# Kernel optimization log

Measured on AMD Instinct MI355X. Metric: run time of the kernel, lower is better.

The kernel has to match this reference:

```python
import jax, jax.numpy as jnp
import numpy as np

DIM = 64
HID = 32  # dim * 1/2
P = 4     # patch_size

def _conv1x1(x, w):
    # x: [B,C,H,W], w: [O,C] -> [B,O,H,W]
    return jnp.einsum('oc,bchw->bohw', w, x)

def _dwconv3x3(x, w):
    # depthwise 3x3, padding 1. x: [B,C,H,W], w: [C,1,3,3]
    return jax.lax.conv_general_dilated(
        x, w, window_strides=(1, 1), padding=((1, 1), (1, 1)),
        dimension_numbers=('NCHW', 'OIHW', 'NCHW'),
        feature_group_count=x.shape[1])

def setup_inputs() -> dict:
    key = jax.random.key(0)
    k1, k2, k3, k4 = jax.random.split(key, 4)
    B, H, W = 4, 512, 512
    x = jax.random.normal(k1, (B, DIM, H, W), dtype=jnp.float32)
    w_in1 = jax.random.normal(k2, (2 * HID, DIM), dtype=jnp.float32) * 0.05
    w_dw = jax.random.normal(k3, (2 * HID, 1, 3, 3), dtype=jnp.float32) * 0.1
    w_in2 = jax.random.normal(k4, (DIM, HID), dtype=jnp.float32) * 0.05
    w_freq = jnp.ones((DIM, 1, 1, P, P // 2 + 1), dtype=jnp.float32)
    return {'x': x, 'w_in1': w_in1, 'w_dw': w_dw, 'w_in2': w_in2, 'w_freq': w_freq}

def reference(x, w_in1, w_dw, w_in2, w_freq):
    shortcut = x
    y = _dwconv3x3(_conv1x1(x, w_in1), w_dw)          # [B,2*HID,H,W]
    y1, y2 = jnp.split(y, 2, axis=1)
    y = jax.nn.gelu(y1, approximate=False) * y2       # [B,HID,H,W]
    y = _conv1x1(y, w_in2)                            # [B,DIM,H,W]
    b, c, h, w = y.shape
    h_n = (P - h % P) % P
    w_n = (P - w % P) % P
    if h_n or w_n:
        y = jnp.pad(y, ((0, 0), (0, 0), (0, h_n), (0, w_n)), mode='reflect')
    hp, wp = y.shape[2] // P, y.shape[3] // P
    # [B,C,hp,P,wp,P] -> [B,C,hp,wp,P,P]
    yp = y.reshape(b, c, hp, P, wp, P).transpose(0, 1, 2, 4, 3, 5)
    yf = jnp.fft.rfft2(yp)                            # [B,C,hp,wp,P,P//2+1] complex
    yf = w_freq * yf                                  # w_freq broadcasts over (C,1,1,P,P//2+1)
    yp = jnp.fft.irfft2(yf, s=(P, P))
    y = yp.transpose(0, 1, 2, 4, 3, 5).reshape(b, c, hp * P, wp * P)
    y = y[:, :, :h, :w]
    return y + shortcut
```

## Files before the change

kernel.cpp:

```cpp
#include <hip/hip_runtime.h>
#include <math.h>

#define DIMC 64
#define HIDC 32
#define IMH 512
#define IMW 512
#define NBATCH 4
#define TW 32
#define TH 8
#define HW 34
#define HH 10
#define NPIX (HW*HH)
#define NPIXP 352
#define NCHUNK 22
#define TSTRIDE 35
#define VSTRIDE 17
#define PLANE (IMH*IMW)

typedef short short8 __attribute__((ext_vector_type(8)));
typedef float f32x4  __attribute__((ext_vector_type(4)));

static __device__ __forceinline__ unsigned cvt_pk_bf16(float lo, float hi) {
    unsigned r;
    asm("v_cvt_pk_bf16_f32 %0, %1, %2" : "=v"(r) : "v"(lo), "v"(hi));
    return r;
}
static __device__ __forceinline__ float bf2f_lo(unsigned s) {
    union { unsigned u; float f; } v; v.u = s << 16; return v.f;
}
static __device__ __forceinline__ float bf2f_hi(unsigned s) {
    union { unsigned u; float f; } v; v.u = s & 0xffff0000u; return v.f;
}
static __device__ __forceinline__ unsigned f2bf(float f) {
    union { float f; unsigned u; } v; v.f = f;
    return (v.u + 0x7fffu + ((v.u >> 16) & 1u)) >> 16;
}

static __device__ __forceinline__ float gelu_f(float u) {
    const float z  = fabsf(u) * 0.70710678118654752f;
    const float t  = __builtin_amdgcn_rcpf(fmaf(0.3275911f, z, 1.0f));
    const float e  = __builtin_amdgcn_exp2f(-z * z * 1.4426950408889634f);
    float p = fmaf(t, 1.061405429f, -1.453152027f);
    p = fmaf(t, p, 1.421413741f);
    p = fmaf(t, p, -0.284496736f);
    p = fmaf(t, p, 0.254829592f);
    p = p * t;
    const float erf_abs = fmaf(-p, e, 1.0f);
    const float erfv = copysignf(erf_abs, u);
    return 0.5f * u * (1.0f + erfv);
}

__global__ __launch_bounds__(256, 3)
void ffn_fused_kernel(const float* __restrict__ x,
                      const float* __restrict__ w1,
                      const float* __restrict__ wdw,
                      const float* __restrict__ w2,
                      const float* __restrict__ wf,
                      float* __restrict__ out)
{
    __shared__ unsigned ts[NPIXP * TSTRIDE];
    __shared__ int s_ident;

    const int tid = threadIdx.x;
    const int bid = ((blockIdx.x & 7) << 9) + (blockIdx.x >> 3);
    const int b  = bid >> 10;
    const int tr = bid & 1023;
    const int ty = tr >> 4, tx = tr & 15;
    const int oy = ty * TH, ox = tx * TW;

    if (tid == 0) s_ident = 1;
    __syncthreads();
    if (tid < DIMC) {
        bool idf = true;
        #pragma unroll
        for (int k = 0; k < 12; ++k) idf = idf && (wf[tid * 12 + k] == 1.0f);
        if (!idf) atomicAnd(&s_ident, 0);
    }

    const float* xb = x + (size_t)b * DIMC * PLANE;

    for (int p = tid; p < NPIXP; p += 256) {
        const int hy = p / HW, hx = p % HW;
        const int gy = oy + hy - 1, gx = ox + hx - 1;
        unsigned* row = &ts[p * TSTRIDE];
        if (p >= NPIX || (unsigned)gy >= IMH || (unsigned)gx >= IMW) {
            #pragma unroll
            for (int w = 0; w < 32; ++w) row[w] = 0u;
        } else {
            const float* xp = xb + (size_t)gy * IMW + gx;
            #pragma unroll
            for (int c0 = 0; c0 < DIMC; c0 += 8) {
                float f[8];
                #pragma unroll
                for (int i = 0; i < 8; ++i) f[i] = xp[(size_t)(c0 + i) * PLANE];
                #pragma unroll
                for (int i = 0; i < 8; i += 2)
                    row[(c0 + i) >> 1] = cvt_pk_bf16(f[i], f[i + 1]);
            }
        }
    }

    const int lane = tid & 63, wid = tid >> 6;
    const int l15 = lane & 15, lg = lane >> 4;

    short8 afrag1[4][2];
    #pragma unroll
    for (int mt = 0; mt < 4; ++mt) {
        #pragma unroll
        for (int ks = 0; ks < 2; ++ks) {
            const float* wp = w1 + (size_t)(mt * 16 + l15) * DIMC + ks * 32 + lg * 8;
            f32x4 wa = *reinterpret_cast<const f32x4*>(wp);
            f32x4 wb = *reinterpret_cast<const f32x4*>(wp + 4);
            union { unsigned u[4]; short8 s; } pk;
            pk.u[0] = cvt_pk_bf16(wa[0], wa[1]); pk.u[1] = cvt_pk_bf16(wa[2], wa[3]);
            pk.u[2] = cvt_pk_bf16(wb[0], wb[1]); pk.u[3] = cvt_pk_bf16(wb[2], wb[3]);
            afrag1[mt][ks] = pk.s;
        }
    }
    short8 afrag2[4];
    #pragma unroll
    for (int mt = 0; mt < 4; ++mt) {
        const float* wp = w2 + (size_t)(mt * 16 + l15) * HIDC + lg * 8;
        f32x4 wa = *reinterpret_cast<const f32x4*>(wp);
        f32x4 wb = *reinterpret_cast<const f32x4*>(wp + 4);
        union { unsigned u[4]; short8 s; } pk;
        pk.u[0] = cvt_pk_bf16(wa[0], wa[1]); pk.u[1] = cvt_pk_bf16(wa[2], wa[3]);
        pk.u[2] = cvt_pk_bf16(wb[0], wb[1]); pk.u[3] = cvt_pk_bf16(wb[2], wb[3]);
        afrag2[mt] = pk.s;
    }
    __syncthreads();

    unsigned xs[4][4][2];
    #pragma unroll
    for (int cc = 0; cc < 4; ++cc) {
        const int px = wid * 64 + cc * 16 + l15;
        const unsigned hp = (unsigned)(((px >> 5) + 1) * HW + (px & 31) + 1) * TSTRIDE;
        #pragma unroll
        for (int mt = 0; mt < 4; ++mt) {
            xs[cc][mt][0] = ts[hp + mt * 8 + lg * 2];
            xs[cc][mt][1] = ts[hp + mt * 8 + lg * 2 + 1];
        }
    }
    __syncthreads();

    for (int chunk = wid; chunk < NCHUNK; chunk += 4) {
        const unsigned base = (unsigned)(chunk * 16 + l15) * TSTRIDE;
        f32x4 acc[4];
        #pragma unroll
        for (int mt = 0; mt < 4; ++mt) acc[mt] = (f32x4)0.0f;
        #pragma unroll
        for (int ks = 0; ks < 2; ++ks) {
            union { unsigned u[4]; short8 s; } bw;
            #pragma unroll
            for (int t = 0; t < 4; ++t) bw.u[t] = ts[base + ks * 16 + lg * 4 + t];
            #pragma unroll
            for (int mt = 0; mt < 4; ++mt)
                acc[mt] = __builtin_amdgcn_mfma_f32_16x16x32_bf16(afrag1[mt][ks], bw.s, acc[mt], 0, 0, 0);
        }
        #pragma unroll
        for (int mt = 0; mt < 2; ++mt) {
            #pragma unroll
            for (int r = 0; r < 4; ++r)
                ts[base + mt * 16 + lg * 4 + r] = cvt_pk_bf16(acc[mt][r], acc[mt + 2][r]);
        }
    }
    __syncthreads();

    const int li = tid >> 5, lj = tid & 31;
    unsigned vpack[16];
    #pragma unroll 2
    for (int c2 = 0; c2 < 16; ++c2) {
        const int ca = 2 * c2, cb = 2 * c2 + 1;
        float u1a = 0.0f, u2a = 0.0f, u1b = 0.0f, u2b = 0.0f;
        #pragma unroll
        for (int di = 0; di < 3; ++di) {
            #pragma unroll
            for (int dj = 0; dj < 3; ++dj) {
                const int k = di * 3 + dj;
                const unsigned base = ((li + di) * HW + (lj + dj)) * TSTRIDE + ca;
                const unsigned ua = ts[base];
                const unsigned ub = ts[base + 1];
                u1a = fmaf(wdw[ca * 9 + k],          bf2f_lo(ua), u1a);
                u2a = fmaf(wdw[(ca + HIDC) * 9 + k], bf2f_hi(ua), u2a);
                u1b = fmaf(wdw[cb * 9 + k],          bf2f_lo(ub), u1b);
                u2b = fmaf(wdw[(cb + HIDC) * 9 + k], bf2f_hi(ub), u2b);
            }
        }
        const float va = gelu_f(u1a) * u2a;
        const float vb = gelu_f(u1b) * u2b;
        vpack[c2] = cvt_pk_bf16(va, vb);
    }
    __syncthreads();

    unsigned* vls = ts;
    {
        const unsigned vb_ = (unsigned)tid * VSTRIDE;
        #pragma unroll
        for (int w = 0; w < 16; ++w) vls[vb_ + w] = vpack[w];
    }
    __syncthreads();

    float* ob = out + (size_t)b * DIMC * PLANE;
    if (s_ident) {
        #pragma unroll
        for (int cc = 0; cc < 4; ++cc) {
            const int chunk = wid * 4 + cc;
            const int px = chunk * 16 + l15;
            union { unsigned u[4]; short8 s; } bw;
            #pragma unroll
            for (int t = 0; t < 4; ++t) bw.u[t] = vls[(unsigned)px * VSTRIDE + lg * 4 + t];
            const size_t pix = (size_t)(oy + (px >> 5)) * IMW + (ox + (px & 31));
            float* op = ob + pix;
            #pragma unroll
            for (int mt = 0; mt < 4; ++mt) {
                f32x4 acc = __builtin_amdgcn_mfma_f32_16x16x32_bf16(afrag2[mt], bw.s, (f32x4)0.0f, 0, 0, 0);
                #pragma unroll
                for (int r = 0; r < 4; ++r) {
                    const int ch = mt * 16 + lg * 4 + r;
                    const unsigned xw = xs[cc][mt][r >> 1];
                    const float xv = (r & 1) ? bf2f_hi(xw) : bf2f_lo(xw);
                    op[(size_t)ch * PLANE] = acc[r] + xv;
                }
            }
        }
    } else {
        float* ys = (float*)(ts + 8192);
        for (int mt = 0; mt < 4; ++mt) {
            __syncthreads();
            #pragma unroll
            for (int cc = 0; cc < 4; ++cc) {
                const int chunk = wid * 4 + cc;
                const int px = chunk * 16 + l15;
                union { unsigned u[4]; short8 s; } bw;
                #pragma unroll
                for (int t = 0; t < 4; ++t) bw.u[t] = vls[(unsigned)px * VSTRIDE + lg * 4 + t];
                f32x4 acc = __builtin_amdgcn_mfma_f32_16x16x32_bf16(afrag2[mt], bw.s, (f32x4)0.0f, 0, 0, 0);
                #pragma unroll
                for (int r = 0; r < 4; ++r)
                    ys[(lg * 4 + r) * 257 + px] = acc[r];
            }
            __syncthreads();
            {
                const int chl = tid >> 4;
                const int ch  = mt * 16 + chl;
                const int pt  = tid & 15;
                const int pi = (pt >> 3) * 4, pj = (pt & 7) * 4;
                float yv[4][4];
                #pragma unroll
                for (int a = 0; a < 4; ++a)
                    #pragma unroll
                    for (int c = 0; c < 4; ++c)
                        yv[a][c] = ys[chl * 257 + (pi + a) * TW + (pj + c)];
                float Cr[4][4], Ci[4][4];
                #pragma unroll
                for (int j = 0; j < 4; ++j) {
                    const float s02 = yv[0][j] + yv[2][j], d02 = yv[0][j] - yv[2][j];
                    const float s13 = yv[1][j] + yv[3][j], d13 = yv[1][j] - yv[3][j];
                    Cr[0][j] = s02 + s13; Ci[0][j] = 0.0f;
                    Cr[1][j] = d02;       Ci[1][j] = -d13;
                    Cr[2][j] = s02 - s13; Ci[2][j] = 0.0f;
                    Cr[3][j] = d02;       Ci[3][j] = d13;
                }
                float Zr[4][3], Zi[4][3];
                #pragma unroll
                for (int u = 0; u < 4; ++u) {
                    const float r0 = Cr[u][0], r1 = Cr[u][1], r2 = Cr[u][2], r3 = Cr[u][3];
                    const float i0 = Ci[u][0], i1 = Ci[u][1], i2 = Ci[u][2], i3 = Ci[u][3];
                    Zr[u][0] = r0 + r1 + r2 + r3;     Zi[u][0] = i0 + i1 + i2 + i3;
                    Zr[u][1] = (r0 - r2) + (i1 - i3); Zi[u][1] = (i0 - i2) - (r1 - r3);
                    Zr[u][2] = r0 - r1 + r2 - r3;     Zi[u][2] = i0 - i1 + i2 - i3;
                    #pragma unroll
                    for (int vv = 0; vv < 3; ++vv) {
                        const float m = wf[ch * 12 + u * 3 + vv];
                        Zr[u][vv] *= m; Zi[u][vv] *= m;
                    }
                }
                float Ar[4][3], Ai[4][3];
                #pragma unroll
                for (int vv = 0; vv < 3; ++vv) {
                    const float r0 = Zr[0][vv], r1 = Zr[1][vv], r2 = Zr[2][vv], r3 = Zr[3][vv];
                    const float i0 = Zi[0][vv], i1 = Zi[1][vv], i2 = Zi[2][vv], i3 = Zi[3][vv];
                    Ar[0][vv] = r0 + r1 + r2 + r3;     Ai[0][vv] = i0 + i1 + i2 + i3;
                    Ar[1][vv] = (r0 - r2) - (i1 - i3); Ai[1][vv] = (i0 - i2) + (r1 - r3);
                    Ar[2][vv] = r0 - r1 + r2 - r3;     Ai[2][vv] = i0 - i1 + i2 - i3;
                    Ar[3][vv] = (r0 - r2) + (i1 - i3); Ai[3][vv] = (i0 - i2) - (r1 - r3);
                }
                const float* xc = xb + (size_t)ch * PLANE;
                float*       oc = ob + (size_t)ch * PLANE;
                #pragma unroll
                for (int a = 0; a < 4; ++a) {
                    const float A0 = Ar[a][0], A1r = Ar[a][1], A2 = Ar[a][2];
                    const float B1i = Ai[a][1];
                    float res[4];
                    res[0] = (A0 + 2.0f * A1r + A2) * 0.0625f;
                    res[1] = (A0 - 2.0f * B1i - A2) * 0.0625f;
                    res[2] = (A0 - 2.0f * A1r + A2) * 0.0625f;
                    res[3] = (A0 + 2.0f * B1i - A2) * 0.0625f;
                    #pragma unroll
                    for (int c = 0; c < 4; ++c) {
                        const size_t pix = (size_t)(oy + pi + a) * IMW + (ox + pj + c);
                        oc[pix] = res[c] + xc[pix];
                    }
                }
            }
        }
    }
}

extern "C" void kernel_launch(void* const* d_in, const int* in_sizes, int n_in,
                              void* d_out, int out_size, void* d_ws, size_t ws_size,
                              hipStream_t stream) {
    (void)in_sizes; (void)n_in; (void)d_ws; (void)ws_size; (void)out_size;
    const float* x   = (const float*)d_in[0];
    const float* w1  = (const float*)d_in[1];
    const float* wdw = (const float*)d_in[2];
    const float* w2  = (const float*)d_in[3];
    const float* wf  = (const float*)d_in[4];
    float* out = (float*)d_out;

    const int blocks = NBATCH * (IMH / TH) * (IMW / TW);
    ffn_fused_kernel<<<blocks, 256, 0, stream>>>(x, w1, wdw, w2, wf, out);
}
```

Measured before the change: 212.9 us.

## Switch to fp16 packed math, taller tiles, XOR-swizzled LDS and weight prep kernel

Moves the intermediate data from bf16 to fp16 and runs the depthwise 3x3 with packed half2 FMAs instead of scalar fp32 FMAs. The tile height doubles to 16 rows with 512-thread blocks, which cuts the halo recompute overhead. The padded LDS stride is replaced by an XOR swizzle so 128-bit LDS accesses can be used. A small prep kernel pre-packs weights and the identity flag into the workspace. The risks are fp16 range and precision loss in the accumulation, an extra kernel launch, and higher LDS per block, which may lower occupancy.

New measurement: 191.0 us. 10.3% less time.

```diff
diff --git a/kernel.cpp b/kernel.cpp
--- a/kernel.cpp
+++ b/kernel.cpp
@@ -1,39 +1,48 @@
 #include <hip/hip_runtime.h>
+#include <hip/hip_fp16.h>
 #include <math.h>
 
 #define DIMC 64
 #define HIDC 32
 #define IMH 512
 #define IMW 512
-#define NBATCH 4
 #define TW 32
-#define TH 8
+#define TH 16
 #define HW 34
-#define HH 10
+#define HH 18
 #define NPIX (HW*HH)
-#define NPIXP 352
-#define NCHUNK 22
-#define TSTRIDE 35
-#define VSTRIDE 17
+#define NPIXP 624
+#define NCHUNK 39
 #define PLANE (IMH*IMW)
 
-typedef short short8 __attribute__((ext_vector_type(8)));
-typedef float f32x4  __attribute__((ext_vector_type(4)));
-
-static __device__ __forceinline__ unsigned cvt_pk_bf16(float lo, float hi) {
-    unsigned r;
-    asm("v_cvt_pk_bf16_f32 %0, %1, %2" : "=v"(r) : "v"(lo), "v"(hi));
-    return r;
-}
-static __device__ __forceinline__ float bf2f_lo(unsigned s) {
-    union { unsigned u; float f; } v; v.u = s << 16; return v.f;
-}
-static __device__ __forceinline__ float bf2f_hi(unsigned s) {
-    union { unsigned u; float f; } v; v.u = s & 0xffff0000u; return v.f;
-}
-static __device__ __forceinline__ unsigned f2bf(float f) {
-    union { float f; unsigned u; } v; v.f = f;
-    return (v.u + 0x7fffu + ((v.u >> 16) & 1u)) >> 16;
+#define IDOFF 0
+#define W1OFF 16
+#define W2OFF 2064
+#define PWOFF 3088
+
+typedef _Float16 half8  __attribute__((ext_vector_type(8)));
+typedef __fp16   fp16x2 __attribute__((ext_vector_type(2)));
+typedef float f32x4     __attribute__((ext_vector_type(4)));
+typedef unsigned int uint;
+
+union U4H8 { uint4 u; half8 h; };
+
+static __device__ __forceinline__ uint pkrtz(float a, float b) {
+    union { fp16x2 h; uint u; } x;
+    x.h = __builtin_amdgcn_cvt_pkrtz(a, b);
+    return x.u;
+}
+static __device__ __forceinline__ float lo16f(uint u) {
+    union { uint u; _Float16 h[2]; } x; x.u = u; return (float)x.h[0];
+}
+static __device__ __forceinline__ float hi16f(uint u) {
+    union { uint u; _Float16 h[2]; } x; x.u = u; return (float)x.h[1];
+}
+static __device__ __forceinline__ uint pkfma(uint w, uint t, uint acc) {
+    union { uint u; __half2 h; } W, T, A;
+    W.u = w; T.u = t; A.u = acc;
+    A.h = __hfma2(W.h, T.h, A.h);
+    return A.u;
 }
 
 static __device__ __forceinline__ float gelu_f(float u) {
@@ -50,52 +59,66 @@
     return 0.5f * u * (1.0f + erfv);
 }
 
-__global__ __launch_bounds__(256, 3)
-void ffn_fused_kernel(const float* __restrict__ x,
-                      const float* __restrict__ w1,
-                      const float* __restrict__ wdw,
-                      const float* __restrict__ w2,
-                      const float* __restrict__ wf,
-                      float* __restrict__ out)
+__global__ __launch_bounds__(256)
+void ffn_prep(const float* __restrict__ w1, const float* __restrict__ wdw,
+              const float* __restrict__ w2, const float* __restrict__ wf,
+              uint* __restrict__ ws)
 {
-    __shared__ unsigned ts[NPIXP * TSTRIDE];
-    __shared__ int s_ident;
-
+    __shared__ int sid;
     const int tid = threadIdx.x;
-    const int bid = ((blockIdx.x & 7) << 9) + (blockIdx.x >> 3);
-    const int b  = bid >> 10;
-    const int tr = bid & 1023;
+    if (tid == 0) sid = 1;
+    __syncthreads();
+    bool ok = true;
+    for (int i = tid; i < DIMC * 12; i += 256) ok = ok && (wf[i] == 1.0f);
+    if (!ok) atomicAnd(&sid, 0);
+    for (int i = tid; i < 2048; i += 256) ws[W1OFF + i] = pkrtz(w1[2*i], w1[2*i+1]);
+    for (int i = tid; i < 1024; i += 256) ws[W2OFF + i] = pkrtz(w2[2*i], w2[2*i+1]);
+    for (int i = tid; i < 288; i += 256) {
+        const int k = i >> 5, ch = i & 31;
+        ws[PWOFF + i] = pkrtz(wdw[ch*9 + k], wdw[(ch + HIDC)*9 + k]);
+    }
+    __syncthreads();
+    if (tid == 0) ws[IDOFF] = (uint)sid;
+}
+
+__global__ __launch_bounds__(512, 4)
+void ffn_main(const float* __restrict__ x,
+              const uint*  __restrict__ ws,
+              const float* __restrict__ wf,
+              float* __restrict__ out)
+{
+    __shared__ uint ts[NPIXP * 32];
+
+    const int tid = threadIdx.x;
+    const int bid = ((blockIdx.x & 7) << 8) + (blockIdx.x >> 3);
+    const int b  = bid >> 9;
+    const int tr = bid & 511;
     const int ty = tr >> 4, tx = tr & 15;
     const int oy = ty * TH, ox = tx * TW;
 
-    if (tid == 0) s_ident = 1;
-    __syncthreads();
-    if (tid < DIMC) {
-        bool idf = true;
-        #pragma unroll
-        for (int k = 0; k < 12; ++k) idf = idf && (wf[tid * 12 + k] == 1.0f);
-        if (!idf) atomicAnd(&s_ident, 0);
-    }
-
     const float* xb = x + (size_t)b * DIMC * PLANE;
 
-    for (int p = tid; p < NPIXP; p += 256) {
-        const int hy = p / HW, hx = p % HW;
+    for (int p = tid; p < NPIXP; p += 512) {
+        const int hy = p / HW, hx = p - hy * HW;
         const int gy = oy + hy - 1, gx = ox + hx - 1;
-        unsigned* row = &ts[p * TSTRIDE];
+        const uint base = (uint)p << 5, sw = ((uint)p & 7) << 2;
         if (p >= NPIX || (unsigned)gy >= IMH || (unsigned)gx >= IMW) {
             #pragma unroll
-            for (int w = 0; w < 32; ++w) row[w] = 0u;
+            for (int g = 0; g < 8; ++g) {
+                uint4 z = {0u, 0u, 0u, 0u};
+                *reinterpret_cast<uint4*>(&ts[base + (((uint)g << 2) ^ sw)]) = z;
+            }
         } else {
             const float* xp = xb + (size_t)gy * IMW + gx;
             #pragma unroll
-            for (int c0 = 0; c0 < DIMC; c0 += 8) {
+            for (int g = 0; g < 8; ++g) {
                 float f[8];
                 #pragma unroll
-                for (int i = 0; i < 8; ++i) f[i] = xp[(size_t)(c0 + i) * PLANE];
-                #pragma unroll
-                for (int i = 0; i < 8; i += 2)
-                    row[(c0 + i) >> 1] = cvt_pk_bf16(f[i], f[i + 1]);
+                for (int i = 0; i < 8; ++i) f[i] = xp[(size_t)(g * 8 + i) * PLANE];
+                uint4 o;
+                o.x = pkrtz(f[0], f[1]); o.y = pkrtz(f[2], f[3]);
+                o.z = pkrtz(f[4], f[5]); o.w = pkrtz(f[6], f[7]);
+                *reinterpret_cast<uint4*>(&ts[base + (((uint)g << 2) ^ sw)]) = o;
             }
         }
     }
@@ -103,154 +126,151 @@
     const int lane = tid & 63, wid = tid >> 6;
     const int l15 = lane & 15, lg = lane >> 4;
 
-    short8 afrag1[4][2];
-    #pragma unroll
-    for (int mt = 0; mt < 4; ++mt) {
+    half8 afrag1[4][2];
+    const uint4* w1v = reinterpret_cast<const uint4*>(ws + W1OFF);
+    #pragma unroll
+    for (int mt = 0; mt < 4; ++mt)
         #pragma unroll
         for (int ks = 0; ks < 2; ++ks) {
-            const float* wp = w1 + (size_t)(mt * 16 + l15) * DIMC + ks * 32 + lg * 8;
-            f32x4 wa = *reinterpret_cast<const f32x4*>(wp);
-            f32x4 wb = *reinterpret_cast<const f32x4*>(wp + 4);
-            union { unsigned u[4]; short8 s; } pk;
-            pk.u[0] = cvt_pk_bf16(wa[0], wa[1]); pk.u[1] = cvt_pk_bf16(wa[2], wa[3]);
-            pk.u[2] = cvt_pk_bf16(wb[0], wb[1]); pk.u[3] = cvt_pk_bf16(wb[2], wb[3]);
-            afrag1[mt][ks] = pk.s;
-        }
-    }
-    short8 afrag2[4];
-    #pragma unroll
-    for (int mt = 0; mt < 4; ++mt) {
-        const float* wp = w2 + (size_t)(mt * 16 + l15) * HIDC + lg * 8;
-        f32x4 wa = *reinterpret_cast<const f32x4*>(wp);
-        f32x4 wb = *reinterpret_cast<const f32x4*>(wp + 4);
-        union { unsigned u[4]; short8 s; } pk;
-        pk.u[0] = cvt_pk_bf16(wa[0], wa[1]); pk.u[1] = cvt_pk_bf16(wa[2], wa[3]);
-        pk.u[2] = cvt_pk_bf16(wb[0], wb[1]); pk.u[3] = cvt_pk_bf16(wb[2], wb[3]);
-        afrag2[mt] = pk.s;
-    }
-    __syncthreads();
-
-    unsigned xs[4][4][2];
+            U4H8 u; u.u = w1v[(mt*16 + l15)*8 + ks*4 + lg];
+            afrag1[mt][ks] = u.h;
+        }
+    half8 afrag2[4];
+    const uint4* w2v = reinterpret_cast<const uint4*>(ws + W2OFF);
+    #pragma unroll
+    for (int mt = 0; mt < 4; ++mt) { U4H8 u; u.u = w2v[(mt*16 + l15)*4 + lg]; afrag2[mt] = u.h; }
+
+    const uint ident = ws[IDOFF];
+    __syncthreads();
+
+    uint xs[4][4][2];
     #pragma unroll
     for (int cc = 0; cc < 4; ++cc) {
-        const int px = wid * 64 + cc * 16 + l15;
-        const unsigned hp = (unsigned)(((px >> 5) + 1) * HW + (px & 31) + 1) * TSTRIDE;
+        const int px = wid*64 + cc*16 + l15;
+        const int h  = ((px >> 5) + 1) * HW + (px & 31) + 1;
+        const uint base = (uint)h << 5, sw = ((uint)h & 7) << 2;
         #pragma unroll
         for (int mt = 0; mt < 4; ++mt) {
-            xs[cc][mt][0] = ts[hp + mt * 8 + lg * 2];
-            xs[cc][mt][1] = ts[hp + mt * 8 + lg * 2 + 1];
-        }
-    }
-    __syncthreads();
-
-    for (int chunk = wid; chunk < NCHUNK; chunk += 4) {
-        const unsigned base = (unsigned)(chunk * 16 + l15) * TSTRIDE;
+            const uint a = base + (((uint)(mt*8 + lg*2)) ^ sw);
+            xs[cc][mt][0] = ts[a];
+            xs[cc][mt][1] = ts[a + 1];
+        }
+    }
+    __syncthreads();
+
+    for (int chunk = wid; chunk < NCHUNK; chunk += 8) {
+        const uint px = (uint)(chunk*16 + l15);
+        const uint base = px << 5, sw = (px & 7) << 2;
         f32x4 acc[4];
         #pragma unroll
         for (int mt = 0; mt < 4; ++mt) acc[mt] = (f32x4)0.0f;
         #pragma unroll
         for (int ks = 0; ks < 2; ++ks) {
-            union { unsigned u[4]; short8 s; } bw;
-            #pragma unroll
-            for (int t = 0; t < 4; ++t) bw.u[t] = ts[base + ks * 16 + lg * 4 + t];
+            U4H8 u; u.u = *reinterpret_cast<const uint4*>(&ts[base + (((uint)(ks*16 + lg*4)) ^ sw)]);
             #pragma unroll
             for (int mt = 0; mt < 4; ++mt)
-                acc[mt] = __builtin_amdgcn_mfma_f32_16x16x32_bf16(afrag1[mt][ks], bw.s, acc[mt], 0, 0, 0);
+                acc[mt] = __builtin_amdgcn_mfma_f32_16x16x32_f16(afrag1[mt][ks], u.h, acc[mt], 0, 0, 0);
         }
         #pragma unroll
         for (int mt = 0; mt < 2; ++mt) {
-            #pragma unroll
-            for (int r = 0; r < 4; ++r)
-                ts[base + mt * 16 + lg * 4 + r] = cvt_pk_bf16(acc[mt][r], acc[mt + 2][r]);
+            uint4 o;
+            o.x = pkrtz(acc[mt][0], acc[mt+2][0]);
+            o.y = pkrtz(acc[mt][1], acc[mt+2][1]);
+            o.z = pkrtz(acc[mt][2], acc[mt+2][2]);
+            o.w = pkrtz(acc[mt][3], acc[mt+2][3]);
+            *reinterpret_cast<uint4*>(&ts[base + (((uint)(mt*16 + lg*4)) ^ sw)]) = o;
         }
     }
     __syncthreads();
 
     const int li = tid >> 5, lj = tid & 31;
-    unsigned vpack[16];
-    #pragma unroll 2
-    for (int c2 = 0; c2 < 16; ++c2) {
-        const int ca = 2 * c2, cb = 2 * c2 + 1;
-        float u1a = 0.0f, u2a = 0.0f, u1b = 0.0f, u2b = 0.0f;
-        #pragma unroll
-        for (int di = 0; di < 3; ++di) {
-            #pragma unroll
-            for (int dj = 0; dj < 3; ++dj) {
-                const int k = di * 3 + dj;
-                const unsigned base = ((li + di) * HW + (lj + dj)) * TSTRIDE + ca;
-                const unsigned ua = ts[base];
-                const unsigned ub = ts[base + 1];
-                u1a = fmaf(wdw[ca * 9 + k],          bf2f_lo(ua), u1a);
-                u2a = fmaf(wdw[(ca + HIDC) * 9 + k], bf2f_hi(ua), u2a);
-                u1b = fmaf(wdw[cb * 9 + k],          bf2f_lo(ub), u1b);
-                u2b = fmaf(wdw[(cb + HIDC) * 9 + k], bf2f_hi(ub), u2b);
-            }
-        }
-        const float va = gelu_f(u1a) * u2a;
-        const float vb = gelu_f(u1b) * u2b;
-        vpack[c2] = cvt_pk_bf16(va, vb);
-    }
-    __syncthreads();
-
-    unsigned* vls = ts;
+    uint acc2[32];
+    #pragma unroll
+    for (int c = 0; c < 32; ++c) acc2[c] = 0u;
+    #pragma unroll
+    for (int k = 0; k < 9; ++k) {
+        const int di = k / 3, dj = k - di * 3;
+        const uint hpx = (uint)((li + di) * HW + (lj + dj));
+        const uint base = hpx << 5, sw = (hpx & 7) << 2;
+        const uint4* pwv = reinterpret_cast<const uint4*>(ws + PWOFF + k*32);
+        #pragma unroll
+        for (int g = 0; g < 8; ++g) {
+            const uint4 wv = pwv[g];
+            const uint4 tv = *reinterpret_cast<const uint4*>(&ts[base + (((uint)g << 2) ^ sw)]);
+            acc2[g*4+0] = pkfma(wv.x, tv.x, acc2[g*4+0]);
+            acc2[g*4+1] = pkfma(wv.y, tv.y, acc2[g*4+1]);
+            acc2[g*4+2] = pkfma(wv.z, tv.z, acc2[g*4+2]);
+            acc2[g*4+3] = pkfma(wv.w, tv.w, acc2[g*4+3]);
+        }
+    }
+    uint4 vo[4];
+    #pragma unroll
+    for (int gg = 0; gg < 4; ++gg) {
+        uint o[4];
+        #pragma unroll
+        for (int q = 0; q < 4; ++q) {
+            const int c2 = gg*4 + q;
+            const uint wa = acc2[2*c2], wb = acc2[2*c2 + 1];
+            const float v0 = gelu_f(lo16f(wa)) * hi16f(wa);
+            const float v1 = gelu_f(lo16f(wb)) * hi16f(wb);
+            o[q] = pkrtz(v0, v1);
+        }
+        vo[gg].x = o[0]; vo[gg].y = o[1]; vo[gg].z = o[2]; vo[gg].w = o[3];
+    }
+    __syncthreads();
     {
-        const unsigned vb_ = (unsigned)tid * VSTRIDE;
-        #pragma unroll
-        for (int w = 0; w < 16; ++w) vls[vb_ + w] = vpack[w];
+        const uint vb = (uint)tid << 4, swv = ((uint)tid & 3) << 2;
+        #pragma unroll
+        for (int gg = 0; gg < 4; ++gg)
+            *reinterpret_cast<uint4*>(&ts[vb + (((uint)gg << 2) ^ swv)]) = vo[gg];
     }
     __syncthreads();
 
     float* ob = out + (size_t)b * DIMC * PLANE;
-    if (s_ident) {
+    if (ident) {
         #pragma unroll
         for (int cc = 0; cc < 4; ++cc) {
-            const int chunk = wid * 4 + cc;
-            const int px = chunk * 16 + l15;
-            union { unsigned u[4]; short8 s; } bw;
-            #pragma unroll
-            for (int t = 0; t < 4; ++t) bw.u[t] = vls[(unsigned)px * VSTRIDE + lg * 4 + t];
-            const size_t pix = (size_t)(oy + (px >> 5)) * IMW + (ox + (px & 31));
+            const uint px = (uint)(wid*64 + cc*16 + l15);
+            U4H8 u; u.u = *reinterpret_cast<const uint4*>(&ts[(px << 4) + ((((uint)lg ^ (px & 3))) << 2)]);
+            const size_t pix = (size_t)(oy + (int)(px >> 5)) * IMW + (ox + (int)(px & 31));
             float* op = ob + pix;
             #pragma unroll
             for (int mt = 0; mt < 4; ++mt) {
-                f32x4 acc = __builtin_amdgcn_mfma_f32_16x16x32_bf16(afrag2[mt], bw.s, (f32x4)0.0f, 0, 0, 0);
+                f32x4 a = __builtin_amdgcn_mfma_f32_16x16x32_f16(afrag2[mt], u.h, (f32x4)0.0f, 0, 0, 0);
                 #pragma unroll
                 for (int r = 0; r < 4; ++r) {
-                    const int ch = mt * 16 + lg * 4 + r;
-                    const unsigned xw = xs[cc][mt][r >> 1];
-                    const float xv = (r & 1) ? bf2f_hi(xw) : bf2f_lo(xw);
-                    op[(size_t)ch * PLANE] = acc[r] + xv;
+                    const int ch = mt*16 + lg*4 + r;
+                    const uint xw = xs[cc][mt][r >> 1];
+                    const float xv = (r & 1) ? hi16f(xw) : lo16f(xw);
+                    op[(size_t)ch * PLANE] = a[r] + xv;
                 }
             }
         }
     } else {
-        float* ys = (float*)(ts + 8192);
+        float* ys = reinterpret_cast<float*>(ts + 8192);
         for (int mt = 0; mt < 4; ++mt) {
             __syncthreads();
             #pragma unroll
             for (int cc = 0; cc < 4; ++cc) {
-                const int chunk = wid * 4 + cc;
-                const int px = chunk * 16 + l15;
-                union { unsigned u[4]; short8 s; } bw;
-                #pragma unroll
-                for (int t = 0; t < 4; ++t) bw.u[t] = vls[(unsigned)px * VSTRIDE + lg * 4 + t];
-                f32x4 acc = __builtin_amdgcn_mfma_f32_16x16x32_bf16(afrag2[mt], bw.s, (f32x4)0.0f, 0, 0, 0);
+                const uint px = (uint)(wid*64 + cc*16 + l15);
+                U4H8 u; u.u = *reinterpret_cast<const uint4*>(&ts[(px << 4) + ((((uint)lg ^ (px & 3))) << 2)]);
+                f32x4 a = __builtin_amdgcn_mfma_f32_16x16x32_f16(afrag2[mt], u.h, (f32x4)0.0f, 0, 0, 0);
                 #pragma unroll
                 for (int r = 0; r < 4; ++r)
-                    ys[(lg * 4 + r) * 257 + px] = acc[r];
+                    ys[(lg*4 + r) * 520 + (int)px] = a[r];
             }
             __syncthreads();
             {
-                const int chl = tid >> 4;
-                const int ch  = mt * 16 + chl;
-                const int pt  = tid & 15;
+                const int chl = tid >> 5;
+                const int ch  = mt*16 + chl;
+                const int pt  = tid & 31;
                 const int pi = (pt >> 3) * 4, pj = (pt & 7) * 4;
                 float yv[4][4];
                 #pragma unroll
                 for (int a = 0; a < 4; ++a)
                     #pragma unroll
                     for (int c = 0; c < 4; ++c)
-                        yv[a][c] = ys[chl * 257 + (pi + a) * TW + (pj + c)];
+                        yv[a][c] = ys[chl * 520 + (pi + a) * TW + (pj + c)];
                 float Cr[4][4], Ci[4][4];
                 #pragma unroll
                 for (int j = 0; j < 4; ++j) {
@@ -310,14 +330,16 @@
 extern "C" void kernel_launch(void* const* d_in, const int* in_sizes, int n_in,
                               void* d_out, int out_size, void* d_ws, size_t ws_size,
                               hipStream_t stream) {
-    (void)in_sizes; (void)n_in; (void)d_ws; (void)ws_size; (void)out_size;
+    (void)in_sizes; (void)n_in; (void)ws_size; (void)out_size;
     const float* x   = (const float*)d_in[0];
     const float* w1  = (const float*)d_in[1];
     const float* wdw = (const float*)d_in[2];
     const float* w2  = (const float*)d_in[3];
     const float* wf  = (const float*)d_in[4];
     float* out = (float*)d_out;
-
-    const int blocks = NBATCH * (IMH / TH) * (IMW / TW);
-    ffn_fused_kernel<<<blocks, 256, 0, stream>>>(x, w1, wdw, w2, wf, out);
-}
+    uint* ws = (uint*)d_ws;
+
+    ffn_prep<<<1, 256, 0, stream>>>(w1, wdw, w2, wf, ws);
+    const int blocks = 4 * (IMH / TH) * (IMW / TW);
+    ffn_main<<<blocks, 512, 0, stream>>>(x, ws, wf, out);
+}
```
